# Performance work log

Measured on AMD Instinct MI355X. Metric: run time of the kernel, lower is better.

Reference implementation:

```python
import jax, jax.numpy as jnp
import numpy as np

N = 1_000_000
H = 128
G = 4096


def setup_inputs() -> dict:
    key = jax.random.key(0)
    k1, k2, k3, k4 = jax.random.split(key, 4)
    x = jax.random.normal(k1, (N, H), dtype=jnp.float32)
    batch = jnp.sort(jax.random.randint(k2, (N,), 0, G, dtype=jnp.int64))
    w1 = jax.random.normal(k3, (H, H), dtype=jnp.float32) * 0.05
    b1 = jnp.zeros((H,), dtype=jnp.float32)
    w2 = jax.random.normal(k4, (H, 1), dtype=jnp.float32) * 0.05
    b2 = jnp.zeros((1,), dtype=jnp.float32)
    return {"x": x, "batch": batch, "w1": w1, "b1": b1, "w2": w2, "b2": b2, "num_graphs": G}


def reference(x, batch, w1, b1, w2, b2, num_graphs):
    # attention MLP: Linear -> Tanh -> Linear(->1)
    s = (jnp.tanh(x @ w1 + b1) @ w2 + b2)[:, 0]  # [N]
    # segmented (per-graph) stable softmax
    smax = jax.ops.segment_max(s, batch, num_segments=num_graphs)  # [G]
    smax = jnp.where(jnp.isfinite(smax), smax, 0.0)  # guard empty graphs
    e = jnp.exp(s - smax[batch])  # [N]
    denom = jax.ops.segment_sum(e, batch, num_segments=num_graphs)  # [G]
    w = e / jnp.where(denom > 0, denom, 1.0)[batch]  # [N]
    # weighted sum pooling per graph -> [G, H]
    pooled = jax.ops.segment_sum(x * w[:, None], batch, num_segments=num_graphs)
    return pooled
```

## Files before the change

kernel.cpp:

```cpp
#include <hip/hip_runtime.h>
#include <math.h>

#define H 128

__device__ __forceinline__ float fast_tanh(float v) {
    float e = __expf(2.0f * v);
    float r = __builtin_amdgcn_rcpf(e + 1.0f);
    return fmaf(-2.0f, r, 1.0f);
}

__global__ __launch_bounds__(256, 3) void k_compute_s(
    const float* __restrict__ x, const float* __restrict__ w1,
    const float* __restrict__ b1, const float* __restrict__ w2,
    const float* __restrict__ b2, float* __restrict__ s, int n)
{
    __shared__ float xs[64 * H];
    __shared__ float w1c[32 * H];
    const int tid = threadIdx.x;
    const int tr = tid >> 5;
    const int tc = tid & 31;
    const long long row0 = (long long)blockIdx.x * 64;

    {
        const float4* xg4 = (const float4*)x;
        float4* xsv = (float4*)xs;
        const long long lim = (long long)n * (H / 4);
        #pragma unroll
        for (int i = 0; i < 8; ++i) {
            int idx = tid + i * 256;
            long long g = row0 * (H / 4) + idx;
            float4 v = {0.f, 0.f, 0.f, 0.f};
            if (g < lim) v = xg4[g];
            xsv[idx] = v;
        }
    }

    float4 acc[8];
    #pragma unroll
    for (int i = 0; i < 8; ++i) acc[i] = {0.f, 0.f, 0.f, 0.f};

    for (int c = 0; c < 4; ++c) {
        __syncthreads();
        {
            const float4* wg = (const float4*)(w1 + 32 * c * H);
            float4* wv4 = (float4*)w1c;
            #pragma unroll
            for (int i = 0; i < 4; ++i) wv4[tid + i * 256] = wg[tid + i * 256];
        }
        __syncthreads();
        const int kbase = 32 * c;
        #pragma unroll 2
        for (int k = 0; k < 32; k += 4) {
            float4 xv[8];
            #pragma unroll
            for (int i = 0; i < 8; ++i)
                xv[i] = *(const float4*)&xs[(8 * tr + i) * H + kbase + k];
            float4 wv[4];
            #pragma unroll
            for (int kk = 0; kk < 4; ++kk)
                wv[kk] = *(const float4*)&w1c[(k + kk) * H + 4 * tc];
            #pragma unroll
            for (int i = 0; i < 8; ++i) {
                acc[i].x = fmaf(xv[i].x, wv[0].x, acc[i].x);
                acc[i].y = fmaf(xv[i].x, wv[0].y, acc[i].y);
                acc[i].z = fmaf(xv[i].x, wv[0].z, acc[i].z);
                acc[i].w = fmaf(xv[i].x, wv[0].w, acc[i].w);
                acc[i].x = fmaf(xv[i].y, wv[1].x, acc[i].x);
                acc[i].y = fmaf(xv[i].y, wv[1].y, acc[i].y);
                acc[i].z = fmaf(xv[i].y, wv[1].z, acc[i].z);
                acc[i].w = fmaf(xv[i].y, wv[1].w, acc[i].w);
                acc[i].x = fmaf(xv[i].z, wv[2].x, acc[i].x);
                acc[i].y = fmaf(xv[i].z, wv[2].y, acc[i].y);
                acc[i].z = fmaf(xv[i].z, wv[2].z, acc[i].z);
                acc[i].w = fmaf(xv[i].z, wv[2].w, acc[i].w);
                acc[i].x = fmaf(xv[i].w, wv[3].x, acc[i].x);
                acc[i].y = fmaf(xv[i].w, wv[3].y, acc[i].y);
                acc[i].z = fmaf(xv[i].w, wv[3].z, acc[i].z);
                acc[i].w = fmaf(xv[i].w, wv[3].w, acc[i].w);
            }
        }
    }

    const float4 b1v = ((const float4*)b1)[tc];
    const float4 w2v = ((const float4*)w2)[tc];
    const float b2v = b2[0];
    float res[8];
    #pragma unroll
    for (int i = 0; i < 8; ++i) {
        float hx = fast_tanh(acc[i].x + b1v.x);
        float hy = fast_tanh(acc[i].y + b1v.y);
        float hz = fast_tanh(acc[i].z + b1v.z);
        float hw = fast_tanh(acc[i].w + b1v.w);
        res[i] = hx * w2v.x + hy * w2v.y + hz * w2v.z + hw * w2v.w;
    }
    #pragma unroll
    for (int off = 16; off; off >>= 1) {
        #pragma unroll
        for (int i = 0; i < 8; ++i) res[i] += __shfl_xor(res[i], off);
    }
    if (tc == 0) {
        #pragma unroll
        for (int i = 0; i < 8; ++i) {
            long long r = row0 + 8 * tr + i;
            if (r < n) s[r] = res[i] + b2v;
        }
    }
}

__global__ void k_offsets(const int* __restrict__ batch, int n, int g_count,
                          int* __restrict__ offs)
{
    int g = blockIdx.x * blockDim.x + threadIdx.x;
    if (g > g_count) return;
    const bool is64 = (batch[n - 1] == 0);
    int lo = 0, hi = n;
    while (lo < hi) {
        int mid = (lo + hi) >> 1;
        int v = is64 ? batch[2 * mid] : batch[mid];
        if (v < g) lo = mid + 1; else hi = mid;
    }
    offs[g] = lo;
}

__global__ void k_stats(const float* __restrict__ s, const int* __restrict__ offs,
                        float* __restrict__ smax, float* __restrict__ sinv)
{
    const int g = blockIdx.x;
    const int lane = threadIdx.x;
    const int start = offs[g], end = offs[g + 1];
    float m = -INFINITY;
    for (int i = start + lane; i < end; i += 64) m = fmaxf(m, s[i]);
    #pragma unroll
    for (int off = 32; off; off >>= 1) m = fmaxf(m, __shfl_xor(m, off));
    if (!(m >= -3.0e38f)) m = 0.0f;
    float d = 0.0f;
    for (int i = start + lane; i < end; i += 64) d += __expf(s[i] - m);
    #pragma unroll
    for (int off = 32; off; off >>= 1) d += __shfl_xor(d, off);
    if (lane == 0) {
        smax[g] = m;
        sinv[g] = (d > 0.0f) ? (1.0f / d) : 1.0f;
    }
}

__global__ __launch_bounds__(256) void k_pool(
    const float* __restrict__ x, const float* __restrict__ s,
    const int* __restrict__ offs, const float* __restrict__ smax,
    const float* __restrict__ sinv, float* __restrict__ out)
{
    const int g = blockIdx.x;
    const int tid = threadIdx.x;
    const int rr = tid >> 5;
    const int c4 = tid & 31;
    const int start = offs[g], end = offs[g + 1];
    const float m = smax[g];
    const float inv = sinv[g];
    float4 acc = {0.f, 0.f, 0.f, 0.f};
    for (int i = start + rr; i < end; i += 8) {
        float w = __expf(s[i] - m) * inv;
        float4 xv = ((const float4*)(x + (size_t)i * H))[c4];
        acc.x = fmaf(w, xv.x, acc.x);
        acc.y = fmaf(w, xv.y, acc.y);
        acc.z = fmaf(w, xv.z, acc.z);
        acc.w = fmaf(w, xv.w, acc.w);
    }
    __shared__ float4 red[8][32];
    red[rr][c4] = acc;
    __syncthreads();
    if (rr == 0) {
        float4 t = red[0][c4];
        #pragma unroll
        for (int j = 1; j < 8; ++j) {
            float4 u = red[j][c4];
            t.x += u.x; t.y += u.y; t.z += u.z; t.w += u.w;
        }
        ((float4*)(out + (size_t)g * H))[c4] = t;
    }
}

extern "C" void kernel_launch(void* const* d_in, const int* in_sizes, int n_in,
                              void* d_out, int out_size, void* d_ws, size_t ws_size,
                              hipStream_t stream)
{
    const float* x     = (const float*)d_in[0];
    const int*   batch = (const int*)d_in[1];
    const float* w1    = (const float*)d_in[2];
    const float* b1    = (const float*)d_in[3];
    const float* w2    = (const float*)d_in[4];
    const float* b2    = (const float*)d_in[5];
    const int n = in_sizes[0] / H;
    const int G = out_size / H;
    float* out = (float*)d_out;

    float* s    = (float*)d_ws;
    float* smax = s + n;
    float* sinv = smax + G;
    int*   offs = (int*)(sinv + G);

    const int tiles = (n + 63) / 64;
    k_compute_s<<<tiles, 256, 0, stream>>>(x, w1, b1, w2, b2, s, n);
    k_offsets<<<(G + 1 + 255) / 256, 256, 0, stream>>>(batch, n, G, offs);
    k_stats<<<G, 64, 0, stream>>>(s, offs, smax, sinv);
    k_pool<<<G, 256, 0, stream>>>(x, s, offs, smax, sinv, out);
}
```

Before: 1.059 ms.

## Compute attention scores with split-bf16 MFMA in a persistent kernel

Replaces the FP32 FMA tiled GEMM for x@w1 with bf16 MFMA instructions. Each operand is split into high and low bf16 parts and three products are accumulated to approximate fp32 accuracy. W1 is converted once per block into swizzled shared memory, and a persistent grid of 1024 blocks loops over 128-row tiles, which amortises the weight load. The split-precision scheme triples the MFMA count and carries a small accuracy risk.

```diff
diff --git a/kernel.cpp b/kernel.cpp
--- a/kernel.cpp
+++ b/kernel.cpp
@@ -2,6 +2,9 @@
 #include <math.h>
 
 #define H 128
+
+typedef float f32x4 __attribute__((ext_vector_type(4)));
+typedef __bf16 bf16x8 __attribute__((ext_vector_type(8)));
 
 __device__ __forceinline__ float fast_tanh(float v) {
     float e = __expf(2.0f * v);
@@ -9,100 +12,113 @@
     return fmaf(-2.0f, r, 1.0f);
 }
 
-__global__ __launch_bounds__(256, 3) void k_compute_s(
+__global__ __launch_bounds__(256, 2) void k_compute_s_mfma(
     const float* __restrict__ x, const float* __restrict__ w1,
     const float* __restrict__ b1, const float* __restrict__ w2,
-    const float* __restrict__ b2, float* __restrict__ s, int n)
-{
-    __shared__ float xs[64 * H];
-    __shared__ float w1c[32 * H];
+    const float* __restrict__ b2, float* __restrict__ s, int n, int ntiles)
+{
+    __shared__ __bf16 wsm[2 * H * H];
+
     const int tid = threadIdx.x;
-    const int tr = tid >> 5;
-    const int tc = tid & 31;
-    const long long row0 = (long long)blockIdx.x * 64;
-
-    {
-        const float4* xg4 = (const float4*)x;
-        float4* xsv = (float4*)xs;
-        const long long lim = (long long)n * (H / 4);
-        #pragma unroll
-        for (int i = 0; i < 8; ++i) {
-            int idx = tid + i * 256;
-            long long g = row0 * (H / 4) + idx;
-            float4 v = {0.f, 0.f, 0.f, 0.f};
-            if (g < lim) v = xg4[g];
-            xsv[idx] = v;
-        }
-    }
-
-    float4 acc[8];
+
+    for (int idx = tid; idx < H * H; idx += 256) {
+        int k = idx >> 7, nn = idx & 127;
+        float v = w1[idx];
+        __bf16 h = (__bf16)v;
+        __bf16 l = (__bf16)(v - (float)h);
+        int c = (k >> 3) ^ (nn & 15);
+        int pos = nn * H + c * 8 + (k & 7);
+        wsm[pos] = h;
+        wsm[H * H + pos] = l;
+    }
+
+    const int wv = tid >> 6;
+    const int lane = tid & 63;
+    const int p = lane & 15;
+    const int q = lane >> 4;
+
+    float b1v[8], w2v[8];
     #pragma unroll
-    for (int i = 0; i < 8; ++i) acc[i] = {0.f, 0.f, 0.f, 0.f};
-
-    for (int c = 0; c < 4; ++c) {
-        __syncthreads();
-        {
-            const float4* wg = (const float4*)(w1 + 32 * c * H);
-            float4* wv4 = (float4*)w1c;
-            #pragma unroll
-            for (int i = 0; i < 4; ++i) wv4[tid + i * 256] = wg[tid + i * 256];
-        }
-        __syncthreads();
-        const int kbase = 32 * c;
-        #pragma unroll 2
-        for (int k = 0; k < 32; k += 4) {
-            float4 xv[8];
-            #pragma unroll
-            for (int i = 0; i < 8; ++i)
-                xv[i] = *(const float4*)&xs[(8 * tr + i) * H + kbase + k];
-            float4 wv[4];
-            #pragma unroll
-            for (int kk = 0; kk < 4; ++kk)
-                wv[kk] = *(const float4*)&w1c[(k + kk) * H + 4 * tc];
-            #pragma unroll
-            for (int i = 0; i < 8; ++i) {
-                acc[i].x = fmaf(xv[i].x, wv[0].x, acc[i].x);
-                acc[i].y = fmaf(xv[i].x, wv[0].y, acc[i].y);
-                acc[i].z = fmaf(xv[i].x, wv[0].z, acc[i].z);
-                acc[i].w = fmaf(xv[i].x, wv[0].w, acc[i].w);
-                acc[i].x = fmaf(xv[i].y, wv[1].x, acc[i].x);
-                acc[i].y = fmaf(xv[i].y, wv[1].y, acc[i].y);
-                acc[i].z = fmaf(xv[i].y, wv[1].z, acc[i].z);
-                acc[i].w = fmaf(xv[i].y, wv[1].w, acc[i].w);
-                acc[i].x = fmaf(xv[i].z, wv[2].x, acc[i].x);
-                acc[i].y = fmaf(xv[i].z, wv[2].y, acc[i].y);
-                acc[i].z = fmaf(xv[i].z, wv[2].z, acc[i].z);
-                acc[i].w = fmaf(xv[i].z, wv[2].w, acc[i].w);
-                acc[i].x = fmaf(xv[i].w, wv[3].x, acc[i].x);
-                acc[i].y = fmaf(xv[i].w, wv[3].y, acc[i].y);
-                acc[i].z = fmaf(xv[i].w, wv[3].z, acc[i].z);
-                acc[i].w = fmaf(xv[i].w, wv[3].w, acc[i].w);
-            }
-        }
-    }
-
-    const float4 b1v = ((const float4*)b1)[tc];
-    const float4 w2v = ((const float4*)w2)[tc];
+    for (int nt = 0; nt < 8; ++nt) {
+        b1v[nt] = b1[nt * 16 + p];
+        w2v[nt] = w2[nt * 16 + p];
+    }
     const float b2v = b2[0];
-    float res[8];
-    #pragma unroll
-    for (int i = 0; i < 8; ++i) {
-        float hx = fast_tanh(acc[i].x + b1v.x);
-        float hy = fast_tanh(acc[i].y + b1v.y);
-        float hz = fast_tanh(acc[i].z + b1v.z);
-        float hw = fast_tanh(acc[i].w + b1v.w);
-        res[i] = hx * w2v.x + hy * w2v.y + hz * w2v.z + hw * w2v.w;
-    }
-    #pragma unroll
-    for (int off = 16; off; off >>= 1) {
-        #pragma unroll
-        for (int i = 0; i < 8; ++i) res[i] += __shfl_xor(res[i], off);
-    }
-    if (tc == 0) {
-        #pragma unroll
-        for (int i = 0; i < 8; ++i) {
-            long long r = row0 + 8 * tr + i;
-            if (r < n) s[r] = res[i] + b2v;
+
+    __syncthreads();
+
+    for (int tile = blockIdx.x; tile < ntiles; tile += (int)gridDim.x) {
+        const long long base = (long long)tile * 128 + wv * 32;
+
+        bf16x8 ah[2][4], al[2][4];
+        #pragma unroll
+        for (int mt = 0; mt < 2; ++mt) {
+            long long r = base + mt * 16 + p;
+            const float4* rp = (const float4*)(x + r * H);
+            const bool ok = (r < (long long)n);
+            #pragma unroll
+            for (int kc = 0; kc < 4; ++kc) {
+                float4 u0 = {0.f, 0.f, 0.f, 0.f}, u1 = {0.f, 0.f, 0.f, 0.f};
+                if (ok) { u0 = rp[kc * 8 + q * 2]; u1 = rp[kc * 8 + q * 2 + 1]; }
+                float vals[8] = {u0.x, u0.y, u0.z, u0.w, u1.x, u1.y, u1.z, u1.w};
+                #pragma unroll
+                for (int j = 0; j < 8; ++j) {
+                    __bf16 h = (__bf16)vals[j];
+                    ah[mt][kc][j] = h;
+                    al[mt][kc][j] = (__bf16)(vals[j] - (float)h);
+                }
+            }
+        }
+
+        f32x4 acc[2][8];
+        #pragma unroll
+        for (int mt = 0; mt < 2; ++mt)
+            #pragma unroll
+            for (int nt = 0; nt < 8; ++nt)
+                acc[mt][nt] = (f32x4){0.f, 0.f, 0.f, 0.f};
+
+        #pragma unroll
+        for (int nt = 0; nt < 8; ++nt) {
+            const int nn = nt * 16 + p;
+            #pragma unroll
+            for (int kc = 0; kc < 4; ++kc) {
+                const int c = (kc * 4 + q) ^ p;
+                const __bf16* bb = &wsm[nn * H + c * 8];
+                bf16x8 bh = *(const bf16x8*)bb;
+                bf16x8 bl = *(const bf16x8*)(bb + H * H);
+                acc[0][nt] = __builtin_amdgcn_mfma_f32_16x16x32_bf16(ah[0][kc], bh, acc[0][nt], 0, 0, 0);
+                acc[1][nt] = __builtin_amdgcn_mfma_f32_16x16x32_bf16(ah[1][kc], bh, acc[1][nt], 0, 0, 0);
+                acc[0][nt] = __builtin_amdgcn_mfma_f32_16x16x32_bf16(al[0][kc], bh, acc[0][nt], 0, 0, 0);
+                acc[1][nt] = __builtin_amdgcn_mfma_f32_16x16x32_bf16(al[1][kc], bh, acc[1][nt], 0, 0, 0);
+                acc[0][nt] = __builtin_amdgcn_mfma_f32_16x16x32_bf16(ah[0][kc], bl, acc[0][nt], 0, 0, 0);
+                acc[1][nt] = __builtin_amdgcn_mfma_f32_16x16x32_bf16(ah[1][kc], bl, acc[1][nt], 0, 0, 0);
+            }
+        }
+
+        #pragma unroll
+        for (int mt = 0; mt < 2; ++mt) {
+            float part[4] = {0.f, 0.f, 0.f, 0.f};
+            #pragma unroll
+            for (int nt = 0; nt < 8; ++nt) {
+                #pragma unroll
+                for (int rg = 0; rg < 4; ++rg) {
+                    float hv = fast_tanh(acc[mt][nt][rg] + b1v[nt]);
+                    part[rg] = fmaf(hv, w2v[nt], part[rg]);
+                }
+            }
+            #pragma unroll
+            for (int off = 1; off < 16; off <<= 1) {
+                #pragma unroll
+                for (int rg = 0; rg < 4; ++rg)
+                    part[rg] += __shfl_xor(part[rg], off);
+            }
+            if (p == 0) {
+                #pragma unroll
+                for (int rg = 0; rg < 4; ++rg) {
+                    long long row = base + mt * 16 + q * 4 + rg;
+                    if (row < (long long)n) s[row] = part[rg] + b2v;
+                }
+            }
         }
     }
 }
@@ -197,8 +213,8 @@
     float* sinv = smax + G;
     int*   offs = (int*)(sinv + G);
 
-    const int tiles = (n + 63) / 64;
-    k_compute_s<<<tiles, 256, 0, stream>>>(x, w1, b1, w2, b2, s, n);
+    const int tiles = (n + 127) / 128;
+    k_compute_s_mfma<<<1024, 256, 0, stream>>>(x, w1, b1, w2, b2, s, n, tiles);
     k_offsets<<<(G + 1 + 255) / 256, 256, 0, stream>>>(batch, n, G, offs);
     k_stats<<<G, 64, 0, stream>>>(s, offs, smax, sinv);
     k_pool<<<G, 256, 0, stream>>>(x, s, offs, smax, sinv, out);
```

Result: faster. 1.029 ms (-2.9%).
